# Performance work log

Measured on AMD Instinct MI355X. Metric: run time of the kernel, lower is better.

The kernel has to match this reference:

```python
import jax, jax.numpy as jnp
import numpy as np

D_MODEL = 512
D_AUX = 64
B, N = 8, 2048


def setup_inputs() -> dict:
    key = jax.random.key(0)
    ks = jax.random.split(key, 12)
    lim = 1.0 / np.sqrt(D_MODEL)  # torch Linear default init scale
    inp = {
        "x": jax.random.normal(ks[0], (B, N, D_MODEL), dtype=jnp.float32),
        "query_aux": jax.random.normal(ks[1], (B, N, D_AUX), dtype=jnp.float32),
        "key_aux": jax.random.normal(ks[2], (B, N, D_AUX), dtype=jnp.float32),
        "adjacency_mask": jax.random.randint(ks[3], (B, N, N), 0, 2, dtype=jnp.int32),
        "merge_coefficients": jnp.float32(0.3),
        "Wq": jax.random.uniform(ks[4], (D_MODEL, D_MODEL), jnp.float32, -lim, lim),
        "bq": jax.random.uniform(ks[5], (D_MODEL,), jnp.float32, -lim, lim),
        "Wk": jax.random.uniform(ks[6], (D_MODEL, D_MODEL), jnp.float32, -lim, lim),
        "bk": jax.random.uniform(ks[7], (D_MODEL,), jnp.float32, -lim, lim),
        "Wv": jax.random.uniform(ks[8], (D_MODEL, D_MODEL), jnp.float32, -lim, lim),
        "bv": jax.random.uniform(ks[9], (D_MODEL,), jnp.float32, -lim, lim),
        "threshold": jnp.float32(0.5),
    }
    return inp


def reference(x, query_aux, key_aux, adjacency_mask, merge_coefficients,
              Wq, bq, Wk, bk, Wv, bv, threshold):
    d_model = x.shape[-1]
    d_aux = key_aux.shape[-1]
    scale = jnp.asarray(d_model, x.dtype) ** 0.5
    scale_aux = jnp.asarray(d_aux, x.dtype) ** 0.5

    q = x @ Wq.T + bq  # [B,N,D]
    k = x @ Wk.T + bk
    v = x @ Wv.T + bv

    scores = jnp.einsum('bnd,bmd->bnm', q, k) / scale  # [B,N,N]
    scores_aux = jnp.einsum('bnd,bmd->bnm', query_aux, key_aux) / scale_aux

    # data-dependent merge: where aux score nonzero AND score above learned threshold
    merge_mask = (scores_aux != 0) & (scores > threshold)
    merged = (1.0 - merge_coefficients) * scores + merge_coefficients * scores_aux
    scores = jnp.where(merge_mask, merged, scores)

    mask_value = jnp.finfo(scores.dtype).min
    scores = jnp.where(adjacency_mask == 0, mask_value, scores)

    weights = jax.nn.softmax(scores, axis=-1)
    return jnp.einsum('bnm,bmd->bnd', weights, v)
```

## Files before the change

kernel.cpp:

```cpp
#include <hip/hip_runtime.h>
#include <cstdint>

#define SEQ    2048
#define DM     512
#define DAUX   64
#define NBATCH 8
#define MASKVAL -3.402823466e38f

typedef _Float16 f16;
typedef __attribute__((ext_vector_type(2))) _Float16 f16x2;
typedef __attribute__((ext_vector_type(4))) _Float16 f16x4;
typedef __attribute__((ext_vector_type(8))) _Float16 f16x8;
typedef __attribute__((ext_vector_type(4))) float fx4;

__device__ __forceinline__ void g2l16(const void* g, void* l) {
  __builtin_amdgcn_global_load_lds(
      (__attribute__((address_space(1))) void*)const_cast<void*>(g),
      (__attribute__((address_space(3))) void*)l, 16, 0, 0);
}

__device__ __forceinline__ void stage_tile(const f16* __restrict__ g0, int rowstride,
                                           f16* lds, int t) {
#pragma unroll
  for (int p = 0; p < 2; ++p) {
    int L = p * 256 + t;
    g2l16(g0 + (size_t)(L >> 2) * rowstride + (L & 3) * 8, lds + L * 8);
  }
}

__device__ __forceinline__ void mfma_chunk3(const f16* __restrict__ Ahi, const f16* __restrict__ Alo,
                                            const f16* __restrict__ Bhi, const f16* __restrict__ Blo,
                                            fx4 acc[4][4], int wm, int wn, int lane) {
  const int r = lane & 15;
  const int q8 = (lane >> 4) * 8;
  f16x8 ah[4], al[4];
#pragma unroll
  for (int it = 0; it < 4; ++it) {
    int row = wm * 64 + it * 16 + r;
    ah[it] = *(const f16x8*)(Ahi + row * 32 + q8);
    al[it] = *(const f16x8*)(Alo + row * 32 + q8);
  }
#pragma unroll
  for (int jt = 0; jt < 4; ++jt) {
    int col = wn * 64 + jt * 16 + r;
    f16x8 bh = *(const f16x8*)(Bhi + col * 32 + q8);
    f16x8 bl = *(const f16x8*)(Blo + col * 32 + q8);
#pragma unroll
    for (int it = 0; it < 4; ++it) {
      acc[it][jt] = __builtin_amdgcn_mfma_f32_16x16x32_f16(ah[it], bh, acc[it][jt], 0, 0, 0);
      acc[it][jt] = __builtin_amdgcn_mfma_f32_16x16x32_f16(ah[it], bl, acc[it][jt], 0, 0, 0);
      acc[it][jt] = __builtin_amdgcn_mfma_f32_16x16x32_f16(al[it], bh, acc[it][jt], 0, 0, 0);
    }
  }
}

__device__ __forceinline__ void split_write(float v, f16* __restrict__ h, f16* __restrict__ l, size_t i) {
  float s = v * 32.0f;
  f16 hi = (f16)s;
  h[i] = hi;
  l[i] = (f16)(s - (float)hi);
}

__global__ __launch_bounds__(256) void convert_split(
    const float* __restrict__ x, const float* __restrict__ Wq,
    const float* __restrict__ Wk, const float* __restrict__ Wv,
    f16* __restrict__ xh, f16* __restrict__ xl,
    f16* __restrict__ Wh, f16* __restrict__ Wl) {
  int idx = blockIdx.x * 256 + threadIdx.x;
  const float* src; f16* dh; f16* dl; size_t off;
  if (idx < 2097152) { src = x; off = (size_t)idx; dh = xh; dl = xl; }
  else {
    int rr = idx - 2097152; int w = rr >> 16; int o = rr & 65535;
    src = (w == 0) ? Wq : (w == 1) ? Wk : Wv;
    off = (size_t)o; dh = Wh + (size_t)w * 262144; dl = Wl + (size_t)w * 262144;
  }
  float4 v = ((const float4*)src)[off];
  size_t e = off * 4;
  split_write(v.x, dh, dl, e);
  split_write(v.y, dh, dl, e + 1);
  split_write(v.z, dh, dl, e + 2);
  split_write(v.w, dh, dl, e + 3);
}

__global__ __launch_bounds__(256) void qkv_mfma(
    const f16* __restrict__ xh, const f16* __restrict__ xl,
    const f16* __restrict__ Wh, const f16* __restrict__ Wl,
    const float* __restrict__ bq, const float* __restrict__ bk, const float* __restrict__ bv,
    f16* __restrict__ qh, f16* __restrict__ ql,
    f16* __restrict__ kh, f16* __restrict__ kl,
    f16* __restrict__ vth, f16* __restrict__ vtl) {
  __shared__ __align__(16) f16 sm[16384];
  f16 *Ahi = sm, *Alo = sm + 4096, *Bhi = sm + 8192, *Blo = sm + 12288;
  const int t = threadIdx.x;
  const int i0 = blockIdx.x * 128;
  const int j0 = blockIdx.y * 128;
  const int z  = blockIdx.z;
  const f16* WhZ = Wh + (size_t)z * 262144;
  const f16* WlZ = Wl + (size_t)z * 262144;
  const int lane = t & 63, wave = t >> 6;
  const int wm = wave >> 1, wn = wave & 1;
  fx4 acc[4][4] = {};
  for (int d0 = 0; d0 < DM; d0 += 32) {
    __syncthreads();
    stage_tile(xh + (size_t)i0 * DM + d0, DM, Ahi, t);
    stage_tile(xl + (size_t)i0 * DM + d0, DM, Alo, t);
    stage_tile(WhZ + (size_t)j0 * DM + d0, DM, Bhi, t);
    stage_tile(WlZ + (size_t)j0 * DM + d0, DM, Blo, t);
    __syncthreads();
    mfma_chunk3(Ahi, Alo, Bhi, Blo, acc, wm, wn, lane);
  }
  const float* bias = (z == 0) ? bq : (z == 1) ? bk : bv;
  const int q4 = (lane >> 4) * 4, r15 = lane & 15;
  if (z < 2) {
    f16* oh = z ? kh : qh;  f16* ol = z ? kl : ql;
#pragma unroll
    for (int jt = 0; jt < 4; ++jt) {
      int j = j0 + wn * 64 + jt * 16 + r15;
      float bj = bias[j];
#pragma unroll
      for (int it = 0; it < 4; ++it) {
        int ib = i0 + wm * 64 + it * 16 + q4;
#pragma unroll
        for (int g = 0; g < 4; ++g) {
          float val = acc[it][jt][g] * (1.0f / 1024.0f) + bj;
          float s = val * 32.0f;
          f16 hi = (f16)s;
          oh[(size_t)(ib + g) * DM + j] = hi;
          ol[(size_t)(ib + g) * DM + j] = (f16)(s - (float)hi);
        }
      }
    }
  } else {
#pragma unroll
    for (int jt = 0; jt < 4; ++jt) {
      int j = j0 + wn * 64 + jt * 16 + r15;
      float bj = bias[j];
#pragma unroll
      for (int it = 0; it < 4; ++it) {
        int ib = i0 + wm * 64 + it * 16 + q4;
        int bb = ib >> 11, nb = ib & 2047;
        f16x4 hv, lv;
#pragma unroll
        for (int g = 0; g < 4; ++g) {
          float val = acc[it][jt][g] * (1.0f / 1024.0f) + bj;
          float s = val * 32.0f;
          f16 hi = (f16)s;
          hv[g] = hi; lv[g] = (f16)(s - (float)hi);
        }
        size_t base = ((size_t)(bb * DM + j)) * SEQ + nb;
        *(f16x4*)(vth + base) = hv;
        *(f16x4*)(vtl + base) = lv;
      }
    }
  }
}

__global__ __launch_bounds__(256) void scores_mfma(
    const f16* __restrict__ qh, const f16* __restrict__ ql,
    const f16* __restrict__ kh, const f16* __restrict__ kl,
    const float* __restrict__ qa, const float* __restrict__ ka,
    const int* __restrict__ adj,
    const float* __restrict__ mc_p, const float* __restrict__ thr_p,
    float* __restrict__ S) {
  __shared__ __align__(16) f16 sm[18432];
  f16 *Ahi = sm, *Alo = sm + 4096, *Bhi = sm + 8192, *Blo = sm + 12288;
  f16 *QAl = sm;
  f16 *KAl = sm + 9216;
  const int t = threadIdx.x;
  const int n0 = blockIdx.x * 128, m0 = blockIdx.y * 128, b = blockIdx.z;
  const int lane = t & 63, wave = t >> 6;
  const int wm = wave >> 1, wn = wave & 1;
  const int r15 = lane & 15, qd = lane >> 4;

  const float* QAb = qa + ((size_t)b * SEQ + n0) * DAUX;
  const float* KAb = ka + ((size_t)b * SEQ + m0) * DAUX;
#pragma unroll
  for (int p = 0; p < 4; ++p) {
    int L8 = p * 256 + t;
    int row = L8 >> 3, c8 = (L8 & 7) * 8;
    float4 u0 = *(const float4*)(QAb + (size_t)row * DAUX + c8);
    float4 u1 = *(const float4*)(QAb + (size_t)row * DAUX + c8 + 4);
    f16x8 hq = {(f16)u0.x,(f16)u0.y,(f16)u0.z,(f16)u0.w,(f16)u1.x,(f16)u1.y,(f16)u1.z,(f16)u1.w};
    *(f16x8*)(QAl + row * 72 + c8) = hq;
    float4 w0 = *(const float4*)(KAb + (size_t)row * DAUX + c8);
    float4 w1 = *(const float4*)(KAb + (size_t)row * DAUX + c8 + 4);
    f16x8 hk = {(f16)w0.x,(f16)w0.y,(f16)w0.z,(f16)w0.w,(f16)w1.x,(f16)w1.y,(f16)w1.z,(f16)w1.w};
    *(f16x8*)(KAl + row * 72 + c8) = hk;
  }
  __syncthreads();
  f16x2 sax[4][4][2];
  {
    const int q8 = qd * 8;
    f16x8 qa_f[4][2], ka_f[4][2];
#pragma unroll
    for (int it = 0; it < 4; ++it) {
      int row = wm * 64 + it * 16 + r15;
      qa_f[it][0] = *(const f16x8*)(QAl + row * 72 + q8);
      qa_f[it][1] = *(const f16x8*)(QAl + row * 72 + 32 + q8);
    }
#pragma unroll
    for (int jt = 0; jt < 4; ++jt) {
      int col = wn * 64 + jt * 16 + r15;
      ka_f[jt][0] = *(const f16x8*)(KAl + col * 72 + q8);
      ka_f[jt][1] = *(const f16x8*)(KAl + col * 72 + 32 + q8);
    }
#pragma unroll
    for (int it = 0; it < 4; ++it)
#pragma unroll
      for (int jt = 0; jt < 4; ++jt) {
        fx4 tmp = {0.f, 0.f, 0.f, 0.f};
        tmp = __builtin_amdgcn_mfma_f32_16x16x32_f16(qa_f[it][0], ka_f[jt][0], tmp, 0, 0, 0);
        tmp = __builtin_amdgcn_mfma_f32_16x16x32_f16(qa_f[it][1], ka_f[jt][1], tmp, 0, 0, 0);
        sax[it][jt][0] = f16x2{(f16)tmp[0], (f16)tmp[1]};
        sax[it][jt][1] = f16x2{(f16)tmp[2], (f16)tmp[3]};
      }
  }
  fx4 acc[4][4] = {};
  const f16* qhB = qh + ((size_t)b * SEQ + n0) * DM;
  const f16* qlB = ql + ((size_t)b * SEQ + n0) * DM;
  const f16* khB = kh + ((size_t)b * SEQ + m0) * DM;
  const f16* klB = kl + ((size_t)b * SEQ + m0) * DM;
  for (int d0 = 0; d0 < DM; d0 += 32) {
    __syncthreads();
    stage_tile(qhB + d0, DM, Ahi, t);
    stage_tile(qlB + d0, DM, Alo, t);
    stage_tile(khB + d0, DM, Bhi, t);
    stage_tile(klB + d0, DM, Blo, t);
    __syncthreads();
    mfma_chunk3(Ahi, Alo, Bhi, Blo, acc, wm, wn, lane);
  }
  const float mc = *mc_p, thr = *thr_p;
  const float invC = 1.0f / (1024.0f * 22.62741699796952f);
#pragma unroll
  for (int it = 0; it < 4; ++it) {
    int rowb = n0 + wm * 64 + it * 16 + qd * 4;
#pragma unroll
    for (int g = 0; g < 4; ++g) {
      size_t rbase = ((size_t)b * SEQ + rowb + g) * SEQ;
#pragma unroll
      for (int jt = 0; jt < 4; ++jt) {
        int col = m0 + wn * 64 + jt * 16 + r15;
        float s = acc[it][jt][g] * invC;
        float sa = (float)sax[it][jt][g >> 1][g & 1] * 0.125f;
        if (sa != 0.0f && s > thr) s = (1.0f - mc) * s + mc * sa;
        if (adj[rbase + col] == 0) s = MASKVAL;
        S[rbase + col] = s;
      }
    }
  }
}

__global__ __launch_bounds__(256) void softmax_p(
    float* __restrict__ S, float* __restrict__ rowsum) {
  const size_t row = blockIdx.x;
  float* Sr = S + row * SEQ;
  const int t = threadIdx.x;
  float4 v0 = *(const float4*)(Sr + t * 8);
  float4 v1 = *(const float4*)(Sr + t * 8 + 4);
  float vals[8] = {v0.x, v0.y, v0.z, v0.w, v1.x, v1.y, v1.z, v1.w};
  float m = vals[0];
#pragma unroll
  for (int i = 1; i < 8; ++i) m = fmaxf(m, vals[i]);
#pragma unroll
  for (int off = 32; off >= 1; off >>= 1) m = fmaxf(m, __shfl_down(m, off, 64));
  __shared__ float wred[4];
  __shared__ float bmax;
  const int wv = t >> 6, ln = t & 63;
  if (ln == 0) wred[wv] = m;
  __syncthreads();
  if (t == 0) bmax = fmaxf(fmaxf(wred[0], wred[1]), fmaxf(wred[2], wred[3]));
  __syncthreads();
  const float mm = bmax;
  float p[8]; float z = 0.f;
#pragma unroll
  for (int i = 0; i < 8; ++i) { p[i] = __expf(vals[i] - mm); z += p[i]; }
#pragma unroll
  for (int off = 32; off >= 1; off >>= 1) z += __shfl_down(z, off, 64);
  __syncthreads();
  if (ln == 0) wred[wv] = z;
  __syncthreads();
  if (t == 0) rowsum[row] = wred[0] + wred[1] + wred[2] + wred[3];
  f16x8 hv, lv;
#pragma unroll
  for (int i = 0; i < 8; ++i) {
    float s = p[i] * 32.0f;
    f16 hi = (f16)s;
    hv[i] = hi; lv[i] = (f16)(s - (float)hi);
  }
  f16* Ph = (f16*)Sr;
  *(f16x8*)(Ph + t * 8) = hv;
  *(f16x8*)(Ph + 2048 + t * 8) = lv;
}

__global__ __launch_bounds__(256) void pv_mfma(
    const float* __restrict__ S, const f16* __restrict__ vth, const f16* __restrict__ vtl,
    const float* __restrict__ rowsum, float* __restrict__ O) {
  __shared__ __align__(16) f16 sm[16384];
  f16 *Phi = sm, *Plo = sm + 4096, *Bhi = sm + 8192, *Blo = sm + 12288;
  const int t = threadIdx.x;
  const int n0 = blockIdx.x * 128;
  const int d0 = blockIdx.y * 128;
  const int b  = blockIdx.z;
  const int lane = t & 63, wave = t >> 6;
  const int wm = wave >> 1, wn = wave & 1;
  fx4 acc[4][4] = {};
  const char* Srow0 = (const char*)(S + ((size_t)b * SEQ + n0) * SEQ);
  const f16* vhB = vth + ((size_t)(b * DM + d0)) * SEQ;
  const f16* vlB = vtl + ((size_t)(b * DM + d0)) * SEQ;
  for (int m0 = 0; m0 < SEQ; m0 += 32) {
    __syncthreads();
#pragma unroll
    for (int p = 0; p < 2; ++p) {
      int L = p * 256 + t;
      const char* g = Srow0 + (size_t)(L >> 2) * 8192 + (size_t)(m0 + (L & 3) * 8) * 2;
      g2l16(g, Phi + L * 8);
      g2l16(g + 4096, Plo + L * 8);
    }
    stage_tile(vhB + m0, SEQ, Bhi, t);
    stage_tile(vlB + m0, SEQ, Blo, t);
    __syncthreads();
    mfma_chunk3(Phi, Plo, Bhi, Blo, acc, wm, wn, lane);
  }
  const int r15 = lane & 15, qd = lane >> 4;
#pragma unroll
  for (int it = 0; it < 4; ++it) {
    int nb = n0 + wm * 64 + it * 16 + qd * 4;
#pragma unroll
    for (int g = 0; g < 4; ++g) {
      float inv = 1.0f / (1024.0f * rowsum[(size_t)b * SEQ + nb + g]);
      size_t obase = ((size_t)b * SEQ + nb + g) * DM;
#pragma unroll
      for (int jt = 0; jt < 4; ++jt) {
        int d = d0 + wn * 64 + jt * 16 + r15;
        O[obase + d] = acc[it][jt][g] * inv;
      }
    }
  }
}

extern "C" void kernel_launch(void* const* d_in, const int* in_sizes, int n_in,
                              void* d_out, int out_size, void* d_ws, size_t ws_size,
                              hipStream_t stream) {
  const float* x   = (const float*)d_in[0];
  const float* qa  = (const float*)d_in[1];
  const float* ka  = (const float*)d_in[2];
  const int*   adj = (const int*)d_in[3];
  const float* mc  = (const float*)d_in[4];
  const float* Wq  = (const float*)d_in[5];
  const float* bq  = (const float*)d_in[6];
  const float* Wk  = (const float*)d_in[7];
  const float* bk  = (const float*)d_in[8];
  const float* Wv  = (const float*)d_in[9];
  const float* bv  = (const float*)d_in[10];
  const float* thr = (const float*)d_in[11];
  float* out = (float*)d_out;

  char* W = (char*)d_ws;
  f16* qh  = (f16*)W;
  f16* ql  = qh + 8388608;
  f16* kh  = ql + 8388608;
  f16* kl  = kh + 8388608;
  f16* vth = kl + 8388608;
  f16* vtl = vth + 8388608;
  float* S = (float*)(W + 100663296);
  float* rowsum = (float*)(W + 100663296 + 134217728);
  f16* xh = (f16*)S;
  f16* xl = xh + 8388608;
  f16* Wh = xl + 8388608;
  f16* Wl = Wh + 786432;

  convert_split<<<8960, 256, 0, stream>>>(x, Wq, Wk, Wv, xh, xl, Wh, Wl);
  qkv_mfma<<<dim3(128, 4, 3), 256, 0, stream>>>(xh, xl, Wh, Wl, bq, bk, bv,
                                                qh, ql, kh, kl, vth, vtl);
  scores_mfma<<<dim3(16, 16, 8), 256, 0, stream>>>(qh, ql, kh, kl, qa, ka, adj, mc, thr, S);
  softmax_p<<<16384, 256, 0, stream>>>(S, rowsum);
  pv_mfma<<<dim3(16, 4, 8), 256, 0, stream>>>(S, vth, vtl, rowsum, out);
}
```

Before: 609.6 us.

## Use single-fp16 V and probabilities, fp16 scores buffer, swizzled 64-wide K tiles

The V projection and the probability-times-V product drop the hi/lo fp16 split and use a single fp16 operand, which cuts the MFMA work and the bytes those stages move. Scores are now stored as fp16 rather than fp32, with -65504 standing in for the mask value, and softmax writes fp16 probabilities scaled by 1024 in place. All GEMM stages stage 64-wide K chunks into an XOR-swizzled LDS layout to reduce bank conflicts and halve the barrier count. The cost is lower precision in scores, probabilities and V, plus larger LDS use per block, which may lower occupancy.

Result: faster. 535.6 us (-12.1%).

```diff
diff --git a/kernel.cpp b/kernel.cpp
--- a/kernel.cpp
+++ b/kernel.cpp
@@ -4,8 +4,6 @@
 #define SEQ    2048
 #define DM     512
 #define DAUX   64
-#define NBATCH 8
-#define MASKVAL -3.402823466e38f
 
 typedef _Float16 f16;
 typedef __attribute__((ext_vector_type(2))) _Float16 f16x2;
@@ -19,46 +17,70 @@
       (__attribute__((address_space(3))) void*)l, 16, 0, 0);
 }
 
-__device__ __forceinline__ void stage_tile(const f16* __restrict__ g0, int rowstride,
-                                           f16* lds, int t) {
-#pragma unroll
-  for (int p = 0; p < 2; ++p) {
+__device__ __forceinline__ void stage64(const f16* __restrict__ g0, int stride,
+                                        f16* lds, int t) {
+#pragma unroll
+  for (int p = 0; p < 4; ++p) {
     int L = p * 256 + t;
-    g2l16(g0 + (size_t)(L >> 2) * rowstride + (L & 3) * 8, lds + L * 8);
-  }
-}
-
-__device__ __forceinline__ void mfma_chunk3(const f16* __restrict__ Ahi, const f16* __restrict__ Alo,
-                                            const f16* __restrict__ Bhi, const f16* __restrict__ Blo,
-                                            fx4 acc[4][4], int wm, int wn, int lane) {
-  const int r = lane & 15;
+    int row = L >> 3;
+    int jp = L & 7;
+    int jl = jp ^ (row & 7);
+    g2l16(g0 + (size_t)row * stride + jl * 8, lds + L * 8);
+  }
+}
+
+__device__ __forceinline__ f16x8 frag64(const f16* lds, int row, int kq) {
+  int jp = (kq >> 3) ^ (row & 7);
+  return *(const f16x8*)(lds + row * 64 + jp * 8);
+}
+
+__device__ __forceinline__ void chunk3(const f16* Ah, const f16* Al,
+                                       const f16* Bh, const f16* Bl,
+                                       fx4 acc[4][4], int wm, int wn, int lane) {
+  const int r15 = lane & 15;
   const int q8 = (lane >> 4) * 8;
-  f16x8 ah[4], al[4];
-#pragma unroll
-  for (int it = 0; it < 4; ++it) {
-    int row = wm * 64 + it * 16 + r;
-    ah[it] = *(const f16x8*)(Ahi + row * 32 + q8);
-    al[it] = *(const f16x8*)(Alo + row * 32 + q8);
-  }
-#pragma unroll
-  for (int jt = 0; jt < 4; ++jt) {
-    int col = wn * 64 + jt * 16 + r;
-    f16x8 bh = *(const f16x8*)(Bhi + col * 32 + q8);
-    f16x8 bl = *(const f16x8*)(Blo + col * 32 + q8);
+#pragma unroll
+  for (int k0 = 0; k0 < 64; k0 += 32) {
+    f16x8 ah[4], al[4];
 #pragma unroll
     for (int it = 0; it < 4; ++it) {
-      acc[it][jt] = __builtin_amdgcn_mfma_f32_16x16x32_f16(ah[it], bh, acc[it][jt], 0, 0, 0);
-      acc[it][jt] = __builtin_amdgcn_mfma_f32_16x16x32_f16(ah[it], bl, acc[it][jt], 0, 0, 0);
-      acc[it][jt] = __builtin_amdgcn_mfma_f32_16x16x32_f16(al[it], bh, acc[it][jt], 0, 0, 0);
-    }
-  }
-}
-
-__device__ __forceinline__ void split_write(float v, f16* __restrict__ h, f16* __restrict__ l, size_t i) {
-  float s = v * 32.0f;
-  f16 hi = (f16)s;
-  h[i] = hi;
-  l[i] = (f16)(s - (float)hi);
+      int row = wm * 64 + it * 16 + r15;
+      ah[it] = frag64(Ah, row, k0 + q8);
+      al[it] = frag64(Al, row, k0 + q8);
+    }
+#pragma unroll
+    for (int jt = 0; jt < 4; ++jt) {
+      int col = wn * 64 + jt * 16 + r15;
+      f16x8 bh = frag64(Bh, col, k0 + q8);
+      f16x8 bl = frag64(Bl, col, k0 + q8);
+#pragma unroll
+      for (int it = 0; it < 4; ++it) {
+        acc[it][jt] = __builtin_amdgcn_mfma_f32_16x16x32_f16(ah[it], bh, acc[it][jt], 0, 0, 0);
+        acc[it][jt] = __builtin_amdgcn_mfma_f32_16x16x32_f16(ah[it], bl, acc[it][jt], 0, 0, 0);
+        acc[it][jt] = __builtin_amdgcn_mfma_f32_16x16x32_f16(al[it], bh, acc[it][jt], 0, 0, 0);
+      }
+    }
+  }
+}
+
+__device__ __forceinline__ void chunk1(const f16* A, const f16* B,
+                                       fx4 acc[4][4], int wm, int wn, int lane) {
+  const int r15 = lane & 15;
+  const int q8 = (lane >> 4) * 8;
+#pragma unroll
+  for (int k0 = 0; k0 < 64; k0 += 32) {
+    f16x8 a[4];
+#pragma unroll
+    for (int it = 0; it < 4; ++it)
+      a[it] = frag64(A, wm * 64 + it * 16 + r15, k0 + q8);
+#pragma unroll
+    for (int jt = 0; jt < 4; ++jt) {
+      f16x8 b = frag64(B, wn * 64 + jt * 16 + r15, k0 + q8);
+#pragma unroll
+      for (int it = 0; it < 4; ++it)
+        acc[it][jt] = __builtin_amdgcn_mfma_f32_16x16x32_f16(a[it], b, acc[it][jt], 0, 0, 0);
+    }
+  }
 }
 
 __global__ __launch_bounds__(256) void convert_split(
@@ -70,16 +92,24 @@
   const float* src; f16* dh; f16* dl; size_t off;
   if (idx < 2097152) { src = x; off = (size_t)idx; dh = xh; dl = xl; }
   else {
-    int rr = idx - 2097152; int w = rr >> 16; int o = rr & 65535;
+    int rr = idx - 2097152;
+    int w = rr >> 16, o = rr & 65535;
     src = (w == 0) ? Wq : (w == 1) ? Wk : Wv;
-    off = (size_t)o; dh = Wh + (size_t)w * 262144; dl = Wl + (size_t)w * 262144;
+    off = (size_t)o;
+    dh = Wh + (size_t)w * 262144; dl = Wl + (size_t)w * 262144;
   }
   float4 v = ((const float4*)src)[off];
-  size_t e = off * 4;
-  split_write(v.x, dh, dl, e);
-  split_write(v.y, dh, dl, e + 1);
-  split_write(v.z, dh, dl, e + 2);
-  split_write(v.w, dh, dl, e + 3);
+  float vv[4] = {v.x, v.y, v.z, v.w};
+  f16x4 hv, lv;
+#pragma unroll
+  for (int i = 0; i < 4; ++i) {
+    float s = vv[i] * 32.0f;
+    f16 hi = (f16)s;
+    hv[i] = hi;
+    lv[i] = (f16)(s - (float)hi);
+  }
+  *(f16x4*)(dh + off * 4) = hv;
+  *(f16x4*)(dl + off * 4) = lv;
 }
 
 __global__ __launch_bounds__(256) void qkv_mfma(
@@ -88,26 +118,34 @@
     const float* __restrict__ bq, const float* __restrict__ bk, const float* __restrict__ bv,
     f16* __restrict__ qh, f16* __restrict__ ql,
     f16* __restrict__ kh, f16* __restrict__ kl,
-    f16* __restrict__ vth, f16* __restrict__ vtl) {
-  __shared__ __align__(16) f16 sm[16384];
-  f16 *Ahi = sm, *Alo = sm + 4096, *Bhi = sm + 8192, *Blo = sm + 12288;
+    f16* __restrict__ vt) {
+  __shared__ __align__(16) f16 sm[32768];
+  f16 *Ah = sm, *Al = sm + 8192, *Bh = sm + 16384, *Bl = sm + 24576;
   const int t = threadIdx.x;
-  const int i0 = blockIdx.x * 128;
-  const int j0 = blockIdx.y * 128;
-  const int z  = blockIdx.z;
+  const int i0 = blockIdx.x * 128, j0 = blockIdx.y * 128, z = blockIdx.z;
   const f16* WhZ = Wh + (size_t)z * 262144;
   const f16* WlZ = Wl + (size_t)z * 262144;
   const int lane = t & 63, wave = t >> 6;
   const int wm = wave >> 1, wn = wave & 1;
   fx4 acc[4][4] = {};
-  for (int d0 = 0; d0 < DM; d0 += 32) {
-    __syncthreads();
-    stage_tile(xh + (size_t)i0 * DM + d0, DM, Ahi, t);
-    stage_tile(xl + (size_t)i0 * DM + d0, DM, Alo, t);
-    stage_tile(WhZ + (size_t)j0 * DM + d0, DM, Bhi, t);
-    stage_tile(WlZ + (size_t)j0 * DM + d0, DM, Blo, t);
-    __syncthreads();
-    mfma_chunk3(Ahi, Alo, Bhi, Blo, acc, wm, wn, lane);
+  if (z < 2) {
+    for (int d0 = 0; d0 < DM; d0 += 64) {
+      __syncthreads();
+      stage64(xh + (size_t)i0 * DM + d0, DM, Ah, t);
+      stage64(xl + (size_t)i0 * DM + d0, DM, Al, t);
+      stage64(WhZ + (size_t)j0 * DM + d0, DM, Bh, t);
+      stage64(WlZ + (size_t)j0 * DM + d0, DM, Bl, t);
+      __syncthreads();
+      chunk3(Ah, Al, Bh, Bl, acc, wm, wn, lane);
+    }
+  } else {
+    for (int d0 = 0; d0 < DM; d0 += 64) {
+      __syncthreads();
+      stage64(xh + (size_t)i0 * DM + d0, DM, Ah, t);
+      stage64(WhZ + (size_t)j0 * DM + d0, DM, Bh, t);
+      __syncthreads();
+      chunk1(Ah, Bh, acc, wm, wn, lane);
+    }
   }
   const float* bias = (z == 0) ? bq : (z == 1) ? bk : bv;
   const int q4 = (lane >> 4) * 4, r15 = lane & 15;
@@ -139,17 +177,11 @@
       for (int it = 0; it < 4; ++it) {
         int ib = i0 + wm * 64 + it * 16 + q4;
         int bb = ib >> 11, nb = ib & 2047;
-        f16x4 hv, lv;
-#pragma unroll
-        for (int g = 0; g < 4; ++g) {
-          float val = acc[it][jt][g] * (1.0f / 1024.0f) + bj;
-          float s = val * 32.0f;
-          f16 hi = (f16)s;
-          hv[g] = hi; lv[g] = (f16)(s - (float)hi);
-        }
-        size_t base = ((size_t)(bb * DM + j)) * SEQ + nb;
-        *(f16x4*)(vth + base) = hv;
-        *(f16x4*)(vtl + base) = lv;
+        f16x4 hv;
+#pragma unroll
+        for (int g = 0; g < 4; ++g)
+          hv[g] = (f16)(acc[it][jt][g] * (1.0f / 1024.0f) + bj);
+        *(f16x4*)(vt + ((size_t)(bb * DM + j)) * SEQ + nb) = hv;
       }
     }
   }
@@ -161,9 +193,9 @@
     const float* __restrict__ qa, const float* __restrict__ ka,
     const int* __restrict__ adj,
     const float* __restrict__ mc_p, const float* __restrict__ thr_p,
-    float* __restrict__ S) {
-  __shared__ __align__(16) f16 sm[18432];
-  f16 *Ahi = sm, *Alo = sm + 4096, *Bhi = sm + 8192, *Blo = sm + 12288;
+    f16* __restrict__ S16) {
+  __shared__ __align__(16) f16 sm[32768];
+  f16 *Ah = sm, *Al = sm + 8192, *Bh = sm + 16384, *Bl = sm + 24576;
   f16 *QAl = sm;
   f16 *KAl = sm + 9216;
   const int t = threadIdx.x;
@@ -220,14 +252,14 @@
   const f16* qlB = ql + ((size_t)b * SEQ + n0) * DM;
   const f16* khB = kh + ((size_t)b * SEQ + m0) * DM;
   const f16* klB = kl + ((size_t)b * SEQ + m0) * DM;
-  for (int d0 = 0; d0 < DM; d0 += 32) {
+  for (int d0 = 0; d0 < DM; d0 += 64) {
     __syncthreads();
-    stage_tile(qhB + d0, DM, Ahi, t);
-    stage_tile(qlB + d0, DM, Alo, t);
-    stage_tile(khB + d0, DM, Bhi, t);
-    stage_tile(klB + d0, DM, Blo, t);
+    stage64(qhB + d0, DM, Ah, t);
+    stage64(qlB + d0, DM, Al, t);
+    stage64(khB + d0, DM, Bh, t);
+    stage64(klB + d0, DM, Bl, t);
     __syncthreads();
-    mfma_chunk3(Ahi, Alo, Bhi, Blo, acc, wm, wn, lane);
+    chunk3(Ah, Al, Bh, Bl, acc, wm, wn, lane);
   }
   const float mc = *mc_p, thr = *thr_p;
   const float invC = 1.0f / (1024.0f * 22.62741699796952f);
@@ -243,21 +275,22 @@
         float s = acc[it][jt][g] * invC;
         float sa = (float)sax[it][jt][g >> 1][g & 1] * 0.125f;
         if (sa != 0.0f && s > thr) s = (1.0f - mc) * s + mc * sa;
-        if (adj[rbase + col] == 0) s = MASKVAL;
-        S[rbase + col] = s;
+        if (adj[rbase + col] == 0) s = -65504.0f;
+        S16[rbase + col] = (f16)s;
       }
     }
   }
 }
 
 __global__ __launch_bounds__(256) void softmax_p(
-    float* __restrict__ S, float* __restrict__ rowsum) {
+    f16* __restrict__ S16, float* __restrict__ rowsum) {
   const size_t row = blockIdx.x;
-  float* Sr = S + row * SEQ;
+  f16* Sr = S16 + row * SEQ;
   const int t = threadIdx.x;
-  float4 v0 = *(const float4*)(Sr + t * 8);
-  float4 v1 = *(const float4*)(Sr + t * 8 + 4);
-  float vals[8] = {v0.x, v0.y, v0.z, v0.w, v1.x, v1.y, v1.z, v1.w};
+  f16x8 v = *(const f16x8*)(Sr + t * 8);
+  float vals[8];
+#pragma unroll
+  for (int i = 0; i < 8; ++i) vals[i] = (float)v[i];
   float m = vals[0];
 #pragma unroll
   for (int i = 1; i < 8; ++i) m = fmaxf(m, vals[i]);
@@ -271,55 +304,41 @@
   if (t == 0) bmax = fmaxf(fmaxf(wred[0], wred[1]), fmaxf(wred[2], wred[3]));
   __syncthreads();
   const float mm = bmax;
-  float p[8]; float z = 0.f;
-#pragma unroll
-  for (int i = 0; i < 8; ++i) { p[i] = __expf(vals[i] - mm); z += p[i]; }
+  f16x8 p16;
+  float z = 0.f;
+#pragma unroll
+  for (int i = 0; i < 8; ++i) {
+    f16 p = (f16)(__expf(vals[i] - mm) * 1024.0f);
+    p16[i] = p;
+    z += (float)p;
+  }
 #pragma unroll
   for (int off = 32; off >= 1; off >>= 1) z += __shfl_down(z, off, 64);
   __syncthreads();
   if (ln == 0) wred[wv] = z;
   __syncthreads();
   if (t == 0) rowsum[row] = wred[0] + wred[1] + wred[2] + wred[3];
-  f16x8 hv, lv;
-#pragma unroll
-  for (int i = 0; i < 8; ++i) {
-    float s = p[i] * 32.0f;
-    f16 hi = (f16)s;
-    hv[i] = hi; lv[i] = (f16)(s - (float)hi);
-  }
-  f16* Ph = (f16*)Sr;
-  *(f16x8*)(Ph + t * 8) = hv;
-  *(f16x8*)(Ph + 2048 + t * 8) = lv;
+  *(f16x8*)(Sr + t * 8) = p16;
 }
 
 __global__ __launch_bounds__(256) void pv_mfma(
-    const float* __restrict__ S, const f16* __restrict__ vth, const f16* __restrict__ vtl,
+    const f16* __restrict__ P16, const f16* __restrict__ vt,
     const float* __restrict__ rowsum, float* __restrict__ O) {
   __shared__ __align__(16) f16 sm[16384];
-  f16 *Phi = sm, *Plo = sm + 4096, *Bhi = sm + 8192, *Blo = sm + 12288;
+  f16 *Ps = sm, *Vs = sm + 8192;
   const int t = threadIdx.x;
-  const int n0 = blockIdx.x * 128;
-  const int d0 = blockIdx.y * 128;
-  const int b  = blockIdx.z;
+  const int n0 = blockIdx.x * 128, d0 = blockIdx.y * 128, b = blockIdx.z;
   const int lane = t & 63, wave = t >> 6;
   const int wm = wave >> 1, wn = wave & 1;
   fx4 acc[4][4] = {};
-  const char* Srow0 = (const char*)(S + ((size_t)b * SEQ + n0) * SEQ);
-  const f16* vhB = vth + ((size_t)(b * DM + d0)) * SEQ;
-  const f16* vlB = vtl + ((size_t)(b * DM + d0)) * SEQ;
-  for (int m0 = 0; m0 < SEQ; m0 += 32) {
+  const f16* Pb = P16 + ((size_t)b * SEQ + n0) * SEQ;
+  const f16* Vb = vt + ((size_t)b * DM + d0) * SEQ;
+  for (int m0 = 0; m0 < SEQ; m0 += 64) {
     __syncthreads();
-#pragma unroll
-    for (int p = 0; p < 2; ++p) {
-      int L = p * 256 + t;
-      const char* g = Srow0 + (size_t)(L >> 2) * 8192 + (size_t)(m0 + (L & 3) * 8) * 2;
-      g2l16(g, Phi + L * 8);
-      g2l16(g + 4096, Plo + L * 8);
-    }
-    stage_tile(vhB + m0, SEQ, Bhi, t);
-    stage_tile(vlB + m0, SEQ, Blo, t);
+    stage64(Pb + m0, SEQ, Ps, t);
+    stage64(Vb + m0, SEQ, Vs, t);
     __syncthreads();
-    mfma_chunk3(Phi, Plo, Bhi, Blo, acc, wm, wn, lane);
+    chunk1(Ps, Vs, acc, wm, wn, lane);
   }
   const int r15 = lane & 15, qd = lane >> 4;
 #pragma unroll
@@ -327,7 +346,7 @@
     int nb = n0 + wm * 64 + it * 16 + qd * 4;
 #pragma unroll
     for (int g = 0; g < 4; ++g) {
-      float inv = 1.0f / (1024.0f * rowsum[(size_t)b * SEQ + nb + g]);
+      float inv = 1.0f / rowsum[(size_t)b * SEQ + nb + g];
       size_t obase = ((size_t)b * SEQ + nb + g) * DM;
 #pragma unroll
       for (int jt = 0; jt < 4; ++jt) {
@@ -355,24 +374,23 @@
   const float* thr = (const float*)d_in[11];
   float* out = (float*)d_out;
 
-  char* W = (char*)d_ws;
-  f16* qh  = (f16*)W;
+  f16* qh  = (f16*)d_ws;
   f16* ql  = qh + 8388608;
   f16* kh  = ql + 8388608;
   f16* kl  = kh + 8388608;
-  f16* vth = kl + 8388608;
-  f16* vtl = vth + 8388608;
-  float* S = (float*)(W + 100663296);
-  float* rowsum = (float*)(W + 100663296 + 134217728);
-  f16* xh = (f16*)S;
+  f16* vt  = kl + 8388608;
+  f16* S16 = vt + 8388608;
+  float* rowsum = (float*)(S16 + 33554432);
+  f16* xh = S16;
   f16* xl = xh + 8388608;
   f16* Wh = xl + 8388608;
   f16* Wl = Wh + 786432;
 
   convert_split<<<8960, 256, 0, stream>>>(x, Wq, Wk, Wv, xh, xl, Wh, Wl);
   qkv_mfma<<<dim3(128, 4, 3), 256, 0, stream>>>(xh, xl, Wh, Wl, bq, bk, bv,
-                                                qh, ql, kh, kl, vth, vtl);
-  scores_mfma<<<dim3(16, 16, 8), 256, 0, stream>>>(qh, ql, kh, kl, qa, ka, adj, mc, thr, S);
-  softmax_p<<<16384, 256, 0, stream>>>(S, rowsum);
-  pv_mfma<<<dim3(16, 4, 8), 256, 0, stream>>>(S, vth, vtl, rowsum, out);
-}
+                                                qh, ql, kh, kl, vt);
+  scores_mfma<<<dim3(16, 16, 8), 256, 0, stream>>>(qh, ql, kh, kl, qa, ka, adj,
+                                                   mc, thr, S16);
+  softmax_p<<<16384, 256, 0, stream>>>(S16, rowsum);
+  pv_mfma<<<dim3(16, 4, 8), 256, 0, stream>>>(S16, vt, rowsum, out);
+}
```
